# Performance work log

Measured on AMD Instinct MI355X. Metric: run time of the kernel, lower is better.

Reference implementation:

```python
import jax, jax.numpy as jnp
import numpy as np

B, N, P = 64, 800000, 128          # batch, total CpG features, n_pathways (capsules)
H1, H2, C = 256, 128, 32           # MLP hidden_topology and n_output
EPS = 1e-5                         # BatchNorm1d eps


def _xavier(key, fan_in, fan_out, shape):
    bound = np.sqrt(6.0 / (fan_in + fan_out))
    return jax.random.uniform(key, shape, jnp.float32, -bound, bound)


def setup_inputs() -> dict:
    key = jax.random.key(0)
    ks = jax.random.split(key, 10)
    x = jax.random.normal(ks[0], (B, N), jnp.float32)
    # idx: sorted pathway assignment, equal capsule sizes N//P (matches module_lens)
    idx = jnp.sort(jax.random.randint(ks[1], (N,), 0, P)).astype(jnp.int64)
    # SPWModulesLayer.weight: xavier_uniform on shape (1, N)
    w = _xavier(ks[2], N, 1, (N,))
    co_w = jax.random.uniform(ks[3], (P,), jnp.float32, 0.0, 4.0)  # CancelOut init
    bn0_g, bn0_b = jnp.ones(P, jnp.float32), jnp.zeros(P, jnp.float32)
    W1, b1 = _xavier(ks[4], P, H1, (P, H1)), jnp.zeros(H1, jnp.float32)
    bn1_g, bn1_b = jnp.ones(H1, jnp.float32), jnp.zeros(H1, jnp.float32)
    W2, b2 = _xavier(ks[5], H1, H2, (H1, H2)), jnp.zeros(H2, jnp.float32)
    bn2_g, bn2_b = jnp.ones(H2, jnp.float32), jnp.zeros(H2, jnp.float32)
    Wo, bo = _xavier(ks[6], H2, C, (H2, C)), jnp.zeros(C, jnp.float32)
    return {"x": x, "w": w, "co_w": co_w,
            "bn0_g": bn0_g, "bn0_b": bn0_b,
            "W1": W1, "b1": b1, "bn1_g": bn1_g, "bn1_b": bn1_b,
            "W2": W2, "b2": b2, "bn2_g": bn2_g, "bn2_b": bn2_b,
            "Wo": Wo, "bo": bo, "idx": idx}


def _bn(z, g, b):
    # BatchNorm1d in training mode: batch mean, biased variance
    m = jnp.mean(z, axis=0)
    v = jnp.mean((z - m) ** 2, axis=0)
    return (z - m) * jax.lax.rsqrt(v + EPS) * g + b


def reference(x, w, co_w, bn0_g, bn0_b, W1, b1, bn1_g, bn1_b,
              W2, b2, bn2_g, bn2_b, Wo, bo, idx):
    # --- SPWModulesLayer: weighted scatter_add over pathway index (last dim) ---
    WX = jnp.zeros((x.shape[0], P), x.dtype).at[:, idx].add(x * w)   # [B, P]
    Z = _bn(jax.nn.relu(WX), bn0_g, bn0_b)                           # ReLU + BN
    Z = Z * jax.nn.sigmoid(co_w)                                     # CancelOut
    # --- MLP head: Linear->ReLU->BN twice, then Linear->Softmax ---
    h = _bn(jax.nn.relu(Z @ W1 + b1), bn1_g, bn1_b)
    h = _bn(jax.nn.relu(h @ W2 + b2), bn2_g, bn2_b)
    y = jax.nn.softmax(h @ Wo + bo, axis=-1)
    return (y, Z)
```

## Files before the change

### kernel.cpp

```cpp
#include <hip/hip_runtime.h>
#include <hip/hip_bf16.h>
#include <type_traits>

#define BB     64
#define NF4    200000
#define CHUNKS 3125
#define NP     128
#define NH1    256
#define NH2    128
#define NC     32
#define EPSV   1e-5f

typedef float fx4 __attribute__((ext_vector_type(4)));

#define AS_G __attribute__((address_space(1)))
#define AS_L __attribute__((address_space(3)))

__device__ __forceinline__ float dot4(fx4 a, fx4 b) {
    return fmaf(a[0], b[0], fmaf(a[1], b[1], fmaf(a[2], b[2], a[3] * b[3])));
}

template <int N, int I = 0, typename F>
__device__ __forceinline__ void static_for(F&& f) {
    if constexpr (I < N) {
        f(std::integral_constant<int, I>{});
        static_for<N, I + 1>(f);
    }
}

__device__ __forceinline__ int bitrev5(int l) {
    return ((l & 1) << 4) | ((l & 2) << 2) | (l & 4) | ((l & 8) >> 2) | ((l & 16) >> 4);
}

template <int C, int M>
__device__ __forceinline__ void red_step(float* v, int lane) {
    const bool hi = (lane & M) != 0;
    #pragma unroll
    for (int j = 0; j < C / 2; ++j) {
        float mine  = hi ? v[j + C / 2] : v[j];
        float other = hi ? v[j]         : v[j + C / 2];
        v[j] = mine + __shfl_xor(other, M);
    }
}

__device__ __forceinline__ void reduce_emit(float* acc, int lane, int bh,
                                            int path, float* __restrict__ WX) {
    red_step<32, 1>(acc, lane);
    red_step<16, 2>(acc, lane);
    red_step<8,  4>(acc, lane);
    red_step<4,  8>(acc, lane);
    red_step<2, 16>(acc, lane);
    float s = acc[0];
    s += __shfl_xor(s, 32);
    if (lane < 32)
        atomicAdd(&WX[(bh + bitrev5(lane)) * NP + path], s);
}

__global__ __launch_bounds__(64) void k_scatter(
    const float* __restrict__ x, const float* __restrict__ w,
    const int* __restrict__ idx, float* __restrict__ WX)
{
    __shared__ fx4 lds4[32 * 64];
    const int lane = threadIdx.x;
    const int wid  = blockIdx.x;
    const int ch   = wid >> 1;
    const int bh   = (wid & 1) << 5;
    const int n4   = ch * 64 + lane;

    const fx4*  __restrict__ w4 = reinterpret_cast<const fx4*>(w);
    const int4* __restrict__ p4 = reinterpret_cast<const int4*>(idx);
    const fx4*  __restrict__ x4 = reinterpret_cast<const fx4*>(x);

    const fx4  wv = w4[n4];
    const int4 pv = p4[n4];
    const int  pLo = __builtin_amdgcn_readfirstlane(pv.x);
    const int  pHi = __shfl(pv.w, 63);
    const bool uniform = (pLo == pHi);

    fx4 wLo, wHi;
    wLo[0] = (pv.x == pLo) ? wv[0] : 0.f;  wHi[0] = (pv.x == pHi) ? wv[0] : 0.f;
    wLo[1] = (pv.y == pLo) ? wv[1] : 0.f;  wHi[1] = (pv.y == pHi) ? wv[1] : 0.f;
    wLo[2] = (pv.z == pLo) ? wv[2] : 0.f;  wHi[2] = (pv.z == pHi) ? wv[2] : 0.f;
    wLo[3] = (pv.w == pLo) ? wv[3] : 0.f;  wHi[3] = (pv.w == pHi) ? wv[3] : 0.f;

    static_for<32>([&](auto I) {
        constexpr int i = I.value;
        const float* gp = (const float*)(x4 + ((size_t)(bh + i) * NF4 + n4));
        __builtin_amdgcn_global_load_lds((const AS_G float*)gp,
                                         (AS_L float*)(lds4 + i * 64), 16, 0, 0);
    });
    asm volatile("s_waitcnt vmcnt(0)" ::: "memory");

    if (uniform) {
        float acc[32];
        static_for<32>([&](auto I) {
            constexpr int i = I.value;
            acc[i] = dot4(lds4[i * 64 + lane], wLo);
        });
        reduce_emit(acc, lane, bh, pLo, WX);
    } else {
        float acc[32], accH[32];
        static_for<32>([&](auto I) {
            constexpr int i = I.value;
            const fx4 xr = lds4[i * 64 + lane];
            acc[i]  = dot4(xr, wLo);
            accH[i] = dot4(xr, wHi);
        });
        reduce_emit(acc,  lane, bh, pLo, WX);
        reduce_emit(accH, lane, bh, pHi, WX);
    }
}

__global__ void k_zero(float* __restrict__ WX)
{
    const int i = blockIdx.x * 256 + threadIdx.x;
    if (i < BB * NP) WX[i] = 0.f;
}

__device__ __forceinline__ float bn_shfl(float a, float gj, float bj)
{
    float s = a, q = a * a;
    #pragma unroll
    for (int off = 32; off > 0; off >>= 1) {
        s += __shfl_xor(s, off);
        q += __shfl_xor(q, off);
    }
    const float m   = s * (1.f / BB);
    const float var = q * (1.f / BB) - m * m;
    return (a - m) * rsqrtf(var + EPSV) * gj + bj;
}

__global__ __launch_bounds__(256) void k_fc1z(
    const float* __restrict__ WX,   const float* __restrict__ co_w,
    const float* __restrict__ bn0g, const float* __restrict__ bn0b,
    const float* __restrict__ W1,   const float* __restrict__ b1,
    const float* __restrict__ bn1g, const float* __restrict__ bn1b,
    float* __restrict__ Zout, float* __restrict__ h1t)
{
    __shared__ float Zl[NP * 65];
    const int tid  = threadIdx.x;
    const int wv   = tid >> 6;
    const int lane = tid & 63;
    const int blk  = blockIdx.x;

    if (tid < NP) {
        const int p = tid;
        float sum = 0.f, sq = 0.f;
        #pragma unroll 8
        for (int b = 0; b < BB; ++b) {
            const float r = fmaxf(WX[b * NP + p], 0.f);
            sum += r; sq += r * r;
        }
        const float m   = sum * (1.f / BB);
        const float var = sq * (1.f / BB) - m * m;
        const float sc  = rsqrtf(var + EPSV) * bn0g[p];
        const float bt  = bn0b[p];
        const float sig = 1.f / (1.f + expf(-co_w[p]));
        #pragma unroll 8
        for (int b = 0; b < BB; ++b) {
            const float r = fmaxf(WX[b * NP + p], 0.f);
            const float z = ((r - m) * sc + bt) * sig;
            Zl[p * 65 + b] = z;
            if (blk == 0) Zout[b * NP + p] = z;
        }
    }
    __syncthreads();

    const int j = blk * 4 + wv;
    float acc = b1[j];
    #pragma unroll 8
    for (int k = 0; k < NP; ++k)
        acc = fmaf(Zl[k * 65 + lane], W1[k * NH1 + j], acc);
    h1t[j * BB + lane] = bn_shfl(fmaxf(acc, 0.f), bn1g[j], bn1b[j]);
}

template <int K, int NOUT>
__global__ void k_fc_bn_t(const float* __restrict__ in_t,
                          const float* __restrict__ W,
                          const float* __restrict__ bias,
                          const float* __restrict__ g,
                          const float* __restrict__ beta,
                          float* __restrict__ out_t)
{
    const int j = blockIdx.x;
    const int b = threadIdx.x;
    float acc = bias[j];
    #pragma unroll 8
    for (int k = 0; k < K; ++k)
        acc = fmaf(in_t[k * BB + b], W[k * NOUT + j], acc);
    out_t[j * BB + b] = bn_shfl(fmaxf(acc, 0.f), g[j], beta[j]);
}

__global__ void k_head(const float* __restrict__ h2t,
                       const float* __restrict__ Wo,
                       const float* __restrict__ bo,
                       float* __restrict__ y)
{
    const int b = blockIdx.x;
    const int c = threadIdx.x;
    float acc = bo[c];
    #pragma unroll 8
    for (int k = 0; k < NH2; ++k)
        acc = fmaf(h2t[k * BB + b], Wo[k * NC + c], acc);
    float mx = acc;
    #pragma unroll
    for (int off = 16; off > 0; off >>= 1)
        mx = fmaxf(mx, __shfl_xor(mx, off));
    const float e = expf(acc - mx);
    float s = e;
    #pragma unroll
    for (int off = 16; off > 0; off >>= 1)
        s += __shfl_xor(s, off);
    y[b * NC + c] = e / s;
}

extern "C" void kernel_launch(void* const* d_in, const int* in_sizes, int n_in,
                              void* d_out, int out_size, void* d_ws, size_t ws_size,
                              hipStream_t stream)
{
    const float* x    = (const float*)d_in[0];
    const float* w    = (const float*)d_in[1];
    const float* co_w = (const float*)d_in[2];
    const float* bn0g = (const float*)d_in[3];
    const float* bn0b = (const float*)d_in[4];
    const float* W1   = (const float*)d_in[5];
    const float* b1   = (const float*)d_in[6];
    const float* bn1g = (const float*)d_in[7];
    const float* bn1b = (const float*)d_in[8];
    const float* W2   = (const float*)d_in[9];
    const float* b2   = (const float*)d_in[10];
    const float* bn2g = (const float*)d_in[11];
    const float* bn2b = (const float*)d_in[12];
    const float* Wo   = (const float*)d_in[13];
    const float* bo   = (const float*)d_in[14];
    const int*   idx  = (const int*)d_in[15];

    float* out = (float*)d_out;
    float* y   = out;
    float* Z   = out + BB * NC;

    float* WX  = (float*)d_ws;
    float* h1t = WX + BB * NP;
    float* h2t = h1t + BB * NH1;

    k_zero<<<32, 256, 0, stream>>>(WX);
    k_scatter<<<CHUNKS * 2, 64, 0, stream>>>(x, w, idx, WX);
    k_fc1z<<<64, 256, 0, stream>>>(WX, co_w, bn0g, bn0b,
                                   W1, b1, bn1g, bn1b, Z, h1t);
    k_fc_bn_t<NH1, NH2><<<NH2, BB, 0, stream>>>(h1t, W2, b2, bn2g, bn2b, h2t);
    k_head<<<BB, NC, 0, stream>>>(h2t, Wo, bo, y);
}
```

Before: 87.51 us.

## Split scatter block's 32 batch rows across four wavefronts of eight rows

The scatter kernel now launches 256-thread blocks. Each of the four wavefronts loads and reduces 8 batch rows of the chunk instead of one wavefront handling all 32, and the butterfly reduction is shortened to 3 steps plus 3 plain shuffles. The aim is more wavefronts in flight per block and fewer live registers per thread, which should hide memory latency better on this bandwidth-bound pass over x. In exchange, the per-wave weight and index loads are repeated four times and there are four times as many atomics per block, each from fewer lanes.

```diff
diff --git a/kernel.cpp b/kernel.cpp
--- a/kernel.cpp
+++ b/kernel.cpp
@@ -28,8 +28,8 @@
     }
 }
 
-__device__ __forceinline__ int bitrev5(int l) {
-    return ((l & 1) << 4) | ((l & 2) << 2) | (l & 4) | ((l & 8) >> 2) | ((l & 16) >> 4);
+__device__ __forceinline__ int bitrev3(int l) {
+    return ((l & 1) << 2) | (l & 2) | ((l & 4) >> 2);
 }
 
 template <int C, int M>
@@ -43,28 +43,30 @@
     }
 }
 
-__device__ __forceinline__ void reduce_emit(float* acc, int lane, int bh,
-                                            int path, float* __restrict__ WX) {
-    red_step<32, 1>(acc, lane);
-    red_step<16, 2>(acc, lane);
-    red_step<8,  4>(acc, lane);
-    red_step<4,  8>(acc, lane);
-    red_step<2, 16>(acc, lane);
+__device__ __forceinline__ void reduce_emit8(float* acc, int lane, int b0,
+                                             int path, float* __restrict__ WX) {
+    red_step<8, 1>(acc, lane);
+    red_step<4, 2>(acc, lane);
+    red_step<2, 4>(acc, lane);
     float s = acc[0];
+    s += __shfl_xor(s, 8);
+    s += __shfl_xor(s, 16);
     s += __shfl_xor(s, 32);
-    if (lane < 32)
-        atomicAdd(&WX[(bh + bitrev5(lane)) * NP + path], s);
-}
-
-__global__ __launch_bounds__(64) void k_scatter(
+    if (lane < 8)
+        atomicAdd(&WX[(b0 + bitrev3(lane)) * NP + path], s);
+}
+
+__global__ __launch_bounds__(256) void k_scatter(
     const float* __restrict__ x, const float* __restrict__ w,
     const int* __restrict__ idx, float* __restrict__ WX)
 {
     __shared__ fx4 lds4[32 * 64];
-    const int lane = threadIdx.x;
+    const int tid  = threadIdx.x;
+    const int lane = tid & 63;
+    const int wq   = tid >> 6;
     const int wid  = blockIdx.x;
     const int ch   = wid >> 1;
-    const int bh   = (wid & 1) << 5;
+    const int b0   = ((wid & 1) << 5) + wq * 8;
     const int n4   = ch * 64 + lane;
 
     const fx4*  __restrict__ w4 = reinterpret_cast<const fx4*>(w);
@@ -83,31 +85,33 @@
     wLo[2] = (pv.z == pLo) ? wv[2] : 0.f;  wHi[2] = (pv.z == pHi) ? wv[2] : 0.f;
     wLo[3] = (pv.w == pLo) ? wv[3] : 0.f;  wHi[3] = (pv.w == pHi) ? wv[3] : 0.f;
 
-    static_for<32>([&](auto I) {
+    fx4* const myl = lds4 + wq * 8 * 64;
+
+    static_for<8>([&](auto I) {
         constexpr int i = I.value;
-        const float* gp = (const float*)(x4 + ((size_t)(bh + i) * NF4 + n4));
+        const float* gp = (const float*)(x4 + ((size_t)(b0 + i) * NF4 + n4));
         __builtin_amdgcn_global_load_lds((const AS_G float*)gp,
-                                         (AS_L float*)(lds4 + i * 64), 16, 0, 0);
+                                         (AS_L float*)(myl + i * 64), 16, 0, 0);
     });
     asm volatile("s_waitcnt vmcnt(0)" ::: "memory");
 
     if (uniform) {
-        float acc[32];
-        static_for<32>([&](auto I) {
+        float acc[8];
+        static_for<8>([&](auto I) {
             constexpr int i = I.value;
-            acc[i] = dot4(lds4[i * 64 + lane], wLo);
+            acc[i] = dot4(myl[i * 64 + lane], wLo);
         });
-        reduce_emit(acc, lane, bh, pLo, WX);
+        reduce_emit8(acc, lane, b0, pLo, WX);
     } else {
-        float acc[32], accH[32];
-        static_for<32>([&](auto I) {
+        float acc[8], accH[8];
+        static_for<8>([&](auto I) {
             constexpr int i = I.value;
-            const fx4 xr = lds4[i * 64 + lane];
+            const fx4 xr = myl[i * 64 + lane];
             acc[i]  = dot4(xr, wLo);
             accH[i] = dot4(xr, wHi);
         });
-        reduce_emit(acc,  lane, bh, pLo, WX);
-        reduce_emit(accH, lane, bh, pHi, WX);
+        reduce_emit8(acc,  lane, b0, pLo, WX);
+        reduce_emit8(accH, lane, b0, pHi, WX);
     }
 }
 
@@ -244,7 +248,7 @@
     float* h2t = h1t + BB * NH1;
 
     k_zero<<<32, 256, 0, stream>>>(WX);
-    k_scatter<<<CHUNKS * 2, 64, 0, stream>>>(x, w, idx, WX);
+    k_scatter<<<CHUNKS * 2, 256, 0, stream>>>(x, w, idx, WX);
     k_fc1z<<<64, 256, 0, stream>>>(WX, co_w, bn0g, bn0b,
                                    W1, b1, bn1g, bn1b, Z, h1t);
     k_fc_bn_t<NH1, NH2><<<NH2, BB, 0, stream>>>(h1t, W2, b2, bn2g, bn2b, h2t);
```

After: 84.23 us. 1.04x faster.
